# Performance work log

Measured on AMD Instinct MI355X. Metric: run time of the kernel, lower is better.

The kernel has to match this reference:

```python
import jax, jax.numpy as jnp
import numpy as np

K_TOP = 64  # top-k selection size (init kwarg k)


def setup_inputs() -> dict:
    key = jax.random.key(0)
    k1, k2, k3, k4 = jax.random.split(key, 4)
    N, M, D = 512, 100000, 1024
    queries = jax.random.normal(k1, (N, D), dtype=jnp.float32)
    keys = jax.random.normal(k2, (M, D), dtype=jnp.float32)
    values = jax.random.normal(k3, (M, D), dtype=jnp.float32)
    affine = jax.random.normal(k4, (D,), dtype=jnp.float32)  # diag affine param (low_parameter=True)
    return {"queries": queries, "keys": keys, "values": values, "affine": affine}


def reference(queries, keys, values, affine):
    # low_parameter=True -> weight matrix is diag(affine): (queries @ diag(a)) == queries * a
    # scores[n, m] = (queries * affine) @ keys.T ; reduce max over queries dim (dim=0)
    scores = jnp.max(jnp.einsum('nd,md->nm', queries * affine, keys), axis=0)  # [M]
    weights, indices = jax.lax.top_k(scores, K_TOP)            # [k], [k]
    w = jax.nn.softmax(weights)                                # softmax over the k selected scores
    encoding = jnp.sum(w[:, None] * values[indices], axis=0)   # [V]
    return encoding, indices
```

## Files before the change

kernel.cpp:

```cpp
#include <hip/hip_runtime.h>
#include <cstdint>
#include <cstddef>


typedef __attribute__((ext_vector_type(8))) short bf16x8;
typedef __attribute__((ext_vector_type(4))) float f32x4;

static constexpr int NQ = 512;
static constexpr int DD = 1024;
static constexpr int MK = 100000;
static constexpr int BM = 64;
static constexpr int BK = 64;
static constexpr int NKS = DD / BK;
static constexpr int MBLOCKS = (MK + BM - 1) / BM;
static constexpr int CAP = 1024;

static constexpr size_t QSTAGE_OFF   = 0;
static constexpr size_t QSTAGE_BYTES = (size_t)NKS * NQ * 128;
static constexpr size_t SCORES_OFF   = QSTAGE_OFF + QSTAGE_BYTES;
static constexpr size_t SCORES_BYTES = (size_t)MBLOCKS * BM * sizeof(float);
static constexpr size_t CIDX_OFF     = SCORES_OFF + SCORES_BYTES;
static constexpr size_t RESC_OFF     = CIDX_OFF + (size_t)CAP * 4;
static constexpr size_t CNT_OFF      = RESC_OFF + (size_t)CAP * 4;

static constexpr int A_HI = 0;
static constexpr int B_HI = 8192;
static constexpr int GEMM_LDS = 8192 + 65536;

static __device__ __forceinline__ unsigned short f32_to_bf16_rne(float f) {
    unsigned int u = __float_as_uint(f);
    unsigned int r = (u + 0x7FFFu + ((u >> 16) & 1u)) >> 16;
    return (unsigned short)r;
}

static __device__ __forceinline__ unsigned int xform(float f) {
    unsigned int u = __float_as_uint(f);
    return u ^ ((unsigned int)((int)u >> 31) | 0x80000000u);
}
static __device__ __forceinline__ float unxform(unsigned int u) {
    unsigned int b = (u & 0x80000000u) ? (u ^ 0x80000000u) : ~u;
    return __uint_as_float(b);
}

typedef __attribute__((address_space(1))) const unsigned int g1u32;
typedef __attribute__((address_space(3))) unsigned int l3u32;
static __device__ __forceinline__ void async16(const void* g, void* l) {
    __builtin_amdgcn_global_load_lds((g1u32*)g, (l3u32*)(uintptr_t)l, 16, 0, 0);
}

__global__ void prep_q(const float* __restrict__ q, const float* __restrict__ a,
                       unsigned short* __restrict__ qs) {
    int id  = blockIdx.x * 256 + threadIdx.x;
    int p   = id & 7;
    int row = (id >> 3) & (NQ - 1);
    int ks  = id >> 12;
    int c   = p ^ (row & 7);
    int kb  = ks * BK + c * 8;

    const float* qrow = q + (size_t)row * DD + kb;
    float4 v0 = *(const float4*)(qrow);
    float4 v1 = *(const float4*)(qrow + 4);
    float4 a0 = *(const float4*)(a + kb);
    float4 a1 = *(const float4*)(a + kb + 4);
    float f[8] = {v0.x * a0.x, v0.y * a0.y, v0.z * a0.z, v0.w * a0.w,
                  v1.x * a1.x, v1.y * a1.y, v1.z * a1.z, v1.w * a1.w};
    bf16x8 o;
#pragma unroll
    for (int j = 0; j < 8; ++j) o[j] = (short)f32_to_bf16_rne(f[j]);
    *(bf16x8*)(qs + (size_t)id * 8) = o;
}

__launch_bounds__(512, 4)
__global__ void scores_gemm(const float* __restrict__ keys,
                            const unsigned short* __restrict__ qs,
                            float* __restrict__ scores) {
    extern __shared__ char smem[];
    const int tid  = threadIdx.x;
    const int wid  = tid >> 6;
    const int lane = tid & 63;
    const int g    = lane >> 4;
    const int r16  = lane & 15;
    const int m0   = blockIdx.x * BM;

    f32x4 acc[4][4] = {};

    const int arow   = tid >> 3;
    const int acw    = tid & 7;
    const int abyte  = arow * 128 + ((acw ^ (arow & 7)) << 4);
    const bool avalid = (m0 + arow) < MK;
    const float* akey = keys + (size_t)(m0 + arow) * DD + acw * 8;

    char* bhi_dst = smem + B_HI + wid * 8192;
    const char* bsrc = (const char*)qs;

    for (int ks = 0; ks < NKS; ++ks) {
        const char* shi = bsrc + ((size_t)(ks * NQ + wid * 64)) * 128 + lane * 16;
#pragma unroll
        for (int i = 0; i < 8; ++i)
            async16(shi + i * 1024, bhi_dst + i * 1024);

        float f[8];
        if (avalid) {
            float4 v0 = *(const float4*)(akey + (size_t)ks * BK);
            float4 v1 = *(const float4*)(akey + (size_t)ks * BK + 4);
            f[0]=v0.x; f[1]=v0.y; f[2]=v0.z; f[3]=v0.w;
            f[4]=v1.x; f[5]=v1.y; f[6]=v1.z; f[7]=v1.w;
        } else {
#pragma unroll
            for (int j = 0; j < 8; ++j) f[j] = 0.f;
        }
        bf16x8 hi8;
#pragma unroll
        for (int j = 0; j < 8; ++j) hi8[j] = (short)f32_to_bf16_rne(f[j]);
        *(bf16x8*)(smem + A_HI + abyte) = hi8;

        __syncthreads();

#pragma unroll
        for (int s = 0; s < 2; ++s) {
            bf16x8 ah[4], bh[4];
#pragma unroll
            for (int rt = 0; rt < 4; ++rt) {
                int row  = rt * 16 + r16;
                int byte = row * 128 + (((s * 4 + g) ^ (row & 7)) << 4);
                ah[rt] = *(const bf16x8*)(smem + A_HI + byte);
            }
#pragma unroll
            for (int ct = 0; ct < 4; ++ct) {
                int row  = wid * 64 + ct * 16 + r16;
                int byte = row * 128 + (((s * 4 + g) ^ (row & 7)) << 4);
                bh[ct] = *(const bf16x8*)(smem + B_HI + byte);
            }
#pragma unroll
            for (int rt = 0; rt < 4; ++rt)
#pragma unroll
                for (int ct = 0; ct < 4; ++ct)
                    acc[rt][ct] = __builtin_amdgcn_mfma_f32_16x16x32_bf16(ah[rt], bh[ct], acc[rt][ct], 0, 0, 0);
        }
        __syncthreads();
    }

    float* wmax = (float*)smem;
#pragma unroll
    for (int rt = 0; rt < 4; ++rt) {
#pragma unroll
        for (int r = 0; r < 4; ++r) {
            float mx = acc[rt][0][r];
            mx = fmaxf(mx, acc[rt][1][r]);
            mx = fmaxf(mx, acc[rt][2][r]);
            mx = fmaxf(mx, acc[rt][3][r]);
#pragma unroll
            for (int off = 1; off < 16; off <<= 1)
                mx = fmaxf(mx, __shfl_xor(mx, off));
            if (r16 == 0) wmax[wid * 64 + rt * 16 + g * 4 + r] = mx;
        }
    }
    __syncthreads();
    if (tid < BM) {
        float mx = wmax[tid];
#pragma unroll
        for (int w = 1; w < 8; ++w) mx = fmaxf(mx, wmax[w * 64 + tid]);
        int gm = m0 + tid;
        if (gm < MK) scores[gm] = mx;
    }
}

__launch_bounds__(1024)
__global__ void finalize_select(const float* __restrict__ scores,
                                int* __restrict__ cidx, int* __restrict__ cnt) {
    __shared__ unsigned int hist[8192];
    __shared__ unsigned int csum[1024];
    __shared__ int sbT;
    __shared__ int scnt;
    const int tid = threadIdx.x;
    for (int i = tid; i < 8192; i += 1024) hist[i] = 0;
    if (tid == 0) scnt = 0;
    __syncthreads();

    for (int i = tid; i < MK; i += 1024)
        atomicAdd(&hist[xform(scores[i]) >> 19], 1u);
    __syncthreads();

    unsigned int s = 0;
#pragma unroll
    for (int j = 0; j < 8; ++j) s += hist[tid * 8 + j];
    csum[tid] = s;
    __syncthreads();

    if (tid == 0) {
        unsigned int acc = 0;
        int bT = 0;
        for (int cb = 1023; cb >= 0; --cb) {
            unsigned int c = csum[cb];
            if (acc + c >= 64u) {
                for (int b = cb * 8 + 7;; --b) {
                    acc += hist[b];
                    if (acc >= 64u) { bT = b; break; }
                }
                break;
            }
            acc += c;
        }
        sbT = bT;
    }
    __syncthreads();

    const float vlo = unxform((unsigned int)sbT << 19) - 1.0f;
    for (int i = tid; i < MK; i += 1024) {
        if (scores[i] >= vlo) {
            int p = atomicAdd(&scnt, 1);
            if (p < CAP) cidx[p] = i;
        }
    }
    __syncthreads();
    if (tid == 0) cnt[0] = scnt < CAP ? scnt : CAP;
}

__launch_bounds__(256)
__global__ void rescore(const float* __restrict__ q, const float* __restrict__ a,
                        const float* __restrict__ keys,
                        const int* __restrict__ cidx, const int* __restrict__ cnt,
                        float* __restrict__ resc) {
    __shared__ float w[1024];
    __shared__ float smax[4];
    const int b = blockIdx.x;
    if (b >= cnt[0]) return;
    const int m   = cidx[b];
    const int tid = threadIdx.x;

    for (int d = tid; d < 1024; d += 256) w[d] = a[d] * keys[(size_t)m * DD + d];
    __syncthreads();

    const int wid = tid >> 6, lane = tid & 63;
    float best = -__builtin_inff();
    for (int n = wid; n < NQ; n += 4) {
        const float* qr = q + (size_t)n * DD;
        float p = 0.f;
#pragma unroll
        for (int j = 0; j < 4; ++j) {
            float4 v  = *(const float4*)(qr + lane * 4 + 256 * j);
            float4 ww = *(const float4*)(&w[lane * 4 + 256 * j]);
            p += v.x * ww.x + v.y * ww.y + v.z * ww.z + v.w * ww.w;
        }
#pragma unroll
        for (int off = 1; off < 64; off <<= 1) p += __shfl_xor(p, off);
        best = fmaxf(best, p);
    }
    if (lane == 0) smax[wid] = best;
    __syncthreads();
    if (tid == 0)
        resc[b] = fmaxf(fmaxf(smax[0], smax[1]), fmaxf(smax[2], smax[3]));
}

__launch_bounds__(256)
__global__ void final_select(const int* __restrict__ cidx, const float* __restrict__ resc,
                             const int* __restrict__ cnt, const float* __restrict__ values,
                             float* __restrict__ out) {
    __shared__ float selw[64];
    __shared__ int   seli[64];
    const int tid = threadIdx.x;
    int nc = cnt[0];
    if (nc > CAP) nc = CAP;

    if (tid < 64) {
        const int lane = tid;
        float lv[16]; int li[16];
#pragma unroll
        for (int j = 0; j < 16; ++j) {
            int slot = lane + 64 * j;
            bool ok = slot < nc;
            lv[j] = ok ? resc[slot] : -__builtin_inff();
            li[j] = ok ? cidx[slot] : 0x7fffffff;
        }
        for (int it = 0; it < 64; ++it) {
            float bv = -__builtin_inff();
            int bg = 0x7fffffff, bj = 0;
#pragma unroll
            for (int j = 0; j < 16; ++j)
                if (lv[j] > bv || (lv[j] == bv && li[j] < bg)) { bv = lv[j]; bg = li[j]; bj = j; }
            int bcode = (lane << 4) | bj;
#pragma unroll
            for (int off = 1; off < 64; off <<= 1) {
                float ov = __shfl_xor(bv, off);
                int   og = __shfl_xor(bg, off);
                int   oc = __shfl_xor(bcode, off);
                if (ov > bv || (ov == bv && og < bg)) { bv = ov; bg = og; bcode = oc; }
            }
            if ((bcode >> 4) == lane) {
                int wj = bcode & 15;
#pragma unroll
                for (int j = 0; j < 16; ++j) if (j == wj) lv[j] = -__builtin_inff();
            }
            if (lane == 0) { selw[it] = bv; seli[it] = bg; }
        }
    }
    __syncthreads();

    if (tid < 64) {
        float x = selw[tid];
        float mx = x;
#pragma unroll
        for (int off = 1; off < 64; off <<= 1) mx = fmaxf(mx, __shfl_xor(mx, off));
        float e = expf(x - mx);
        float s = e;
#pragma unroll
        for (int off = 1; off < 64; off <<= 1) s += __shfl_xor(s, off);
        selw[tid] = e / s;
        out[DD + tid] = (float)seli[tid];
    }
    __syncthreads();

    for (int d = tid; d < DD; d += 256) {
        float accv = 0.f;
        for (int i = 0; i < 64; ++i)
            accv += selw[i] * values[(size_t)seli[i] * DD + d];
        out[d] = accv;
    }
}

extern "C" void kernel_launch(void* const* d_in, const int* in_sizes, int n_in,
                              void* d_out, int out_size, void* d_ws, size_t ws_size,
                              hipStream_t stream) {
    (void)in_sizes; (void)n_in; (void)out_size; (void)ws_size;
    const float* queries = (const float*)d_in[0];
    const float* keys    = (const float*)d_in[1];
    const float* values  = (const float*)d_in[2];
    const float* affine  = (const float*)d_in[3];
    float* out = (float*)d_out;
    char*  ws  = (char*)d_ws;

    unsigned short* qstage = (unsigned short*)(ws + QSTAGE_OFF);
    float* scores = (float*)(ws + SCORES_OFF);
    int*   cidx   = (int*)(ws + CIDX_OFF);
    float* resc   = (float*)(ws + RESC_OFF);
    int*   cnt    = (int*)(ws + CNT_OFF);

    hipFuncSetAttribute((const void*)scores_gemm,
                        hipFuncAttributeMaxDynamicSharedMemorySize, GEMM_LDS);

    prep_q<<<(NKS * NQ * 8) / 256, 256, 0, stream>>>(queries, affine, qstage);
    scores_gemm<<<MBLOCKS, 512, GEMM_LDS, stream>>>(keys, qstage, scores);
    finalize_select<<<1, 1024, 0, stream>>>(scores, cidx, cnt);
    rescore<<<CAP, 256, 0, stream>>>(queries, affine, keys, cidx, cnt, resc);
    final_select<<<1, 256, 0, stream>>>(cidx, resc, cnt, values, out);
}
```

Measured before the change: 498.0 us.

## Double-buffer score GEMM with prefetch and parallelize top-k threshold selection

The score GEMM halves its K-step to 32, double-buffers both the query tile and the bf16-converted key tile in LDS, and issues the next step's async and global loads before the current MFMAs. This leaves one barrier per step and raises wave priority around the MFMA block. The single-block select kernel is split into separate kernels: zeroing, a multi-block histogram build with global atomics, a parallel suffix-scan threshold search, and a multi-block candidate collect. The intent is to hide load latency in the GEMM and remove the serial one-block pass over 100k scores, at the cost of extra launches and global atomics. The candidate count is no longer clamped to CAP.

```diff
diff --git a/kernel.cpp b/kernel.cpp
--- a/kernel.cpp
+++ b/kernel.cpp
@@ -10,29 +10,30 @@
 static constexpr int DD = 1024;
 static constexpr int MK = 100000;
 static constexpr int BM = 64;
-static constexpr int BK = 64;
+static constexpr int BK = 32;
 static constexpr int NKS = DD / BK;
 static constexpr int MBLOCKS = (MK + BM - 1) / BM;
 static constexpr int CAP = 1024;
 
 static constexpr size_t QSTAGE_OFF   = 0;
-static constexpr size_t QSTAGE_BYTES = (size_t)NKS * NQ * 128;
+static constexpr size_t QSTAGE_BYTES = (size_t)NKS * NQ * 64;
 static constexpr size_t SCORES_OFF   = QSTAGE_OFF + QSTAGE_BYTES;
 static constexpr size_t SCORES_BYTES = (size_t)MBLOCKS * BM * sizeof(float);
 static constexpr size_t CIDX_OFF     = SCORES_OFF + SCORES_BYTES;
 static constexpr size_t RESC_OFF     = CIDX_OFF + (size_t)CAP * 4;
 static constexpr size_t CNT_OFF      = RESC_OFF + (size_t)CAP * 4;
-
-static constexpr int A_HI = 0;
-static constexpr int B_HI = 8192;
-static constexpr int GEMM_LDS = 8192 + 65536;
+static constexpr size_t HIST_OFF     = CNT_OFF + 64;
+static constexpr size_t VLO_OFF      = HIST_OFF + 8192 * 4;
+
+static constexpr int AOFF = 0;
+static constexpr int BOFF = 8192;
+static constexpr int GEMM_LDS = 8192 + 2 * 32768;
 
 static __device__ __forceinline__ unsigned short f32_to_bf16_rne(float f) {
     unsigned int u = __float_as_uint(f);
     unsigned int r = (u + 0x7FFFu + ((u >> 16) & 1u)) >> 16;
     return (unsigned short)r;
 }
-
 static __device__ __forceinline__ unsigned int xform(float f) {
     unsigned int u = __float_as_uint(f);
     return u ^ ((unsigned int)((int)u >> 31) | 0x80000000u);
@@ -40,6 +41,9 @@
 static __device__ __forceinline__ float unxform(unsigned int u) {
     unsigned int b = (u & 0x80000000u) ? (u ^ 0x80000000u) : ~u;
     return __uint_as_float(b);
+}
+static __device__ __forceinline__ int swz4(int row) {
+    return ((row >> 2) ^ row) & 3;
 }
 
 typedef __attribute__((address_space(1))) const unsigned int g1u32;
@@ -51,11 +55,10 @@
 __global__ void prep_q(const float* __restrict__ q, const float* __restrict__ a,
                        unsigned short* __restrict__ qs) {
     int id  = blockIdx.x * 256 + threadIdx.x;
-    int p   = id & 7;
-    int row = (id >> 3) & (NQ - 1);
-    int ks  = id >> 12;
-    int c   = p ^ (row & 7);
-    int kb  = ks * BK + c * 8;
+    int c   = id & 3;
+    int row = (id >> 2) & (NQ - 1);
+    int ks  = id >> 11;
+    int kb  = ks * BK + (c ^ swz4(row)) * 8;
 
     const float* qrow = q + (size_t)row * DD + kb;
     float4 v0 = *(const float4*)(qrow);
@@ -82,63 +85,91 @@
     const int r16  = lane & 15;
     const int m0   = blockIdx.x * BM;
 
+    const int arow = tid >> 3;
+    const int ah   = tid & 7;
+    int srowA = (m0 + arow < MK) ? (m0 + arow) : (MK - 1);
+    const float* aptr = keys + (size_t)srowA * DD + ah * 4;
+    const int awbyte = arow * 64 + ((((ah >> 1) ^ swz4(arow)) & 3) << 4) + (ah & 1) * 8;
+
+    const char* bsrc = (const char*)qs + (size_t)(wid * 64) * 64 + (size_t)lane * 16;
+    const int bdst0 = BOFF + wid * 4096;
+
+    int aoff[4], boff[4];
+#pragma unroll
+    for (int rt = 0; rt < 4; ++rt) {
+        int row = rt * 16 + r16;
+        aoff[rt] = row * 64 + (((g ^ swz4(row)) & 3) << 4);
+    }
+#pragma unroll
+    for (int ct = 0; ct < 4; ++ct) {
+        int row = wid * 64 + ct * 16 + r16;
+        boff[ct] = row * 64 + (((g ^ swz4(row)) & 3) << 4);
+    }
+
     f32x4 acc[4][4] = {};
 
-    const int arow   = tid >> 3;
-    const int acw    = tid & 7;
-    const int abyte  = arow * 128 + ((acw ^ (arow & 7)) << 4);
-    const bool avalid = (m0 + arow) < MK;
-    const float* akey = keys + (size_t)(m0 + arow) * DD + acw * 8;
-
-    char* bhi_dst = smem + B_HI + wid * 8192;
-    const char* bsrc = (const char*)qs;
-
-    for (int ks = 0; ks < NKS; ++ks) {
-        const char* shi = bsrc + ((size_t)(ks * NQ + wid * 64)) * 128 + lane * 16;
-#pragma unroll
-        for (int i = 0; i < 8; ++i)
-            async16(shi + i * 1024, bhi_dst + i * 1024);
-
-        float f[8];
-        if (avalid) {
-            float4 v0 = *(const float4*)(akey + (size_t)ks * BK);
-            float4 v1 = *(const float4*)(akey + (size_t)ks * BK + 4);
-            f[0]=v0.x; f[1]=v0.y; f[2]=v0.z; f[3]=v0.w;
-            f[4]=v1.x; f[5]=v1.y; f[6]=v1.z; f[7]=v1.w;
-        } else {
-#pragma unroll
-            for (int j = 0; j < 8; ++j) f[j] = 0.f;
-        }
-        bf16x8 hi8;
-#pragma unroll
-        for (int j = 0; j < 8; ++j) hi8[j] = (short)f32_to_bf16_rne(f[j]);
-        *(bf16x8*)(smem + A_HI + abyte) = hi8;
-
+#pragma unroll
+    for (int j = 0; j < 4; ++j)
+        async16(bsrc + j * 1024, smem + bdst0 + j * 1024);
+    {
+        float4 a0 = *(const float4*)(aptr);
+        unsigned long long pk =
+            (unsigned long long)f32_to_bf16_rne(a0.x)
+          | ((unsigned long long)f32_to_bf16_rne(a0.y) << 16)
+          | ((unsigned long long)f32_to_bf16_rne(a0.z) << 32)
+          | ((unsigned long long)f32_to_bf16_rne(a0.w) << 48);
+        *(unsigned long long*)(smem + AOFF + awbyte) = pk;
+    }
+    __syncthreads();
+
+    for (int ks = 0; ks < NKS - 1; ++ks) {
+        const int cur = ks & 1, nxt = cur ^ 1;
+#pragma unroll
+        for (int j = 0; j < 4; ++j)
+            async16(bsrc + (size_t)(ks + 1) * 32768 + j * 1024,
+                    smem + bdst0 + nxt * 32768 + j * 1024);
+        float4 an = *(const float4*)(aptr + (ks + 1) * BK);
+
+        bf16x8 ah4[4], bh4[4];
+#pragma unroll
+        for (int rt = 0; rt < 4; ++rt)
+            ah4[rt] = *(const bf16x8*)(smem + AOFF + cur * 4096 + aoff[rt]);
+#pragma unroll
+        for (int ct = 0; ct < 4; ++ct)
+            bh4[ct] = *(const bf16x8*)(smem + BOFF + cur * 32768 + boff[ct]);
+        __builtin_amdgcn_s_setprio(1);
+#pragma unroll
+        for (int rt = 0; rt < 4; ++rt)
+#pragma unroll
+            for (int ct = 0; ct < 4; ++ct)
+                acc[rt][ct] = __builtin_amdgcn_mfma_f32_16x16x32_bf16(ah4[rt], bh4[ct], acc[rt][ct], 0, 0, 0);
+        __builtin_amdgcn_s_setprio(0);
+
+        unsigned long long pk =
+            (unsigned long long)f32_to_bf16_rne(an.x)
+          | ((unsigned long long)f32_to_bf16_rne(an.y) << 16)
+          | ((unsigned long long)f32_to_bf16_rne(an.z) << 32)
+          | ((unsigned long long)f32_to_bf16_rne(an.w) << 48);
+        *(unsigned long long*)(smem + AOFF + nxt * 4096 + awbyte) = pk;
         __syncthreads();
-
-#pragma unroll
-        for (int s = 0; s < 2; ++s) {
-            bf16x8 ah[4], bh[4];
-#pragma unroll
-            for (int rt = 0; rt < 4; ++rt) {
-                int row  = rt * 16 + r16;
-                int byte = row * 128 + (((s * 4 + g) ^ (row & 7)) << 4);
-                ah[rt] = *(const bf16x8*)(smem + A_HI + byte);
-            }
-#pragma unroll
-            for (int ct = 0; ct < 4; ++ct) {
-                int row  = wid * 64 + ct * 16 + r16;
-                int byte = row * 128 + (((s * 4 + g) ^ (row & 7)) << 4);
-                bh[ct] = *(const bf16x8*)(smem + B_HI + byte);
-            }
-#pragma unroll
-            for (int rt = 0; rt < 4; ++rt)
-#pragma unroll
-                for (int ct = 0; ct < 4; ++ct)
-                    acc[rt][ct] = __builtin_amdgcn_mfma_f32_16x16x32_bf16(ah[rt], bh[ct], acc[rt][ct], 0, 0, 0);
-        }
-        __syncthreads();
-    }
+    }
+
+    {
+        const int cur = (NKS - 1) & 1;
+        bf16x8 ah4[4], bh4[4];
+#pragma unroll
+        for (int rt = 0; rt < 4; ++rt)
+            ah4[rt] = *(const bf16x8*)(smem + AOFF + cur * 4096 + aoff[rt]);
+#pragma unroll
+        for (int ct = 0; ct < 4; ++ct)
+            bh4[ct] = *(const bf16x8*)(smem + BOFF + cur * 32768 + boff[ct]);
+#pragma unroll
+        for (int rt = 0; rt < 4; ++rt)
+#pragma unroll
+            for (int ct = 0; ct < 4; ++ct)
+                acc[rt][ct] = __builtin_amdgcn_mfma_f32_16x16x32_bf16(ah4[rt], bh4[ct], acc[rt][ct], 0, 0, 0);
+    }
+    __syncthreads();
 
     float* wmax = (float*)smem;
 #pragma unroll
@@ -165,55 +196,54 @@
     }
 }
 
+__global__ void zero_hist(unsigned int* __restrict__ hist, int* __restrict__ cnt) {
+    int i = blockIdx.x * 1024 + threadIdx.x;
+    if (i < 8192) hist[i] = 0;
+    if (i == 0) cnt[0] = 0;
+}
+
+__global__ void hist_build(const float* __restrict__ scores, unsigned int* __restrict__ hist) {
+    for (int i = blockIdx.x * 256 + threadIdx.x; i < MK; i += gridDim.x * 256)
+        atomicAdd(&hist[xform(scores[i]) >> 19], 1u);
+}
+
 __launch_bounds__(1024)
-__global__ void finalize_select(const float* __restrict__ scores,
-                                int* __restrict__ cidx, int* __restrict__ cnt) {
-    __shared__ unsigned int hist[8192];
-    __shared__ unsigned int csum[1024];
-    __shared__ int sbT;
-    __shared__ int scnt;
+__global__ void find_thresh(const unsigned int* __restrict__ hist, float* __restrict__ vlo) {
+    __shared__ unsigned int s0[1024], s1[1024];
     const int tid = threadIdx.x;
-    for (int i = tid; i < 8192; i += 1024) hist[i] = 0;
-    if (tid == 0) scnt = 0;
-    __syncthreads();
-
-    for (int i = tid; i < MK; i += 1024)
-        atomicAdd(&hist[xform(scores[i]) >> 19], 1u);
-    __syncthreads();
-
     unsigned int s = 0;
 #pragma unroll
     for (int j = 0; j < 8; ++j) s += hist[tid * 8 + j];
-    csum[tid] = s;
-    __syncthreads();
-
-    if (tid == 0) {
-        unsigned int acc = 0;
-        int bT = 0;
-        for (int cb = 1023; cb >= 0; --cb) {
-            unsigned int c = csum[cb];
-            if (acc + c >= 64u) {
-                for (int b = cb * 8 + 7;; --b) {
-                    acc += hist[b];
-                    if (acc >= 64u) { bT = b; break; }
-                }
-                break;
-            }
-            acc += c;
-        }
-        sbT = bT;
-    }
-    __syncthreads();
-
-    const float vlo = unxform((unsigned int)sbT << 19) - 1.0f;
-    for (int i = tid; i < MK; i += 1024) {
-        if (scores[i] >= vlo) {
-            int p = atomicAdd(&scnt, 1);
+    s0[tid] = s;
+    __syncthreads();
+    unsigned int* src = s0;
+    unsigned int* dst = s1;
+    for (int off = 1; off < 1024; off <<= 1) {
+        unsigned int v = src[tid] + ((tid + off < 1024) ? src[tid + off] : 0u);
+        __syncthreads();
+        dst[tid] = v;
+        __syncthreads();
+        unsigned int* t = src; src = dst; dst = t;
+    }
+    unsigned int suf  = src[tid];
+    unsigned int sufn = (tid < 1023) ? src[tid + 1] : 0u;
+    if (suf >= 64u && sufn < 64u) {
+        unsigned int acc = sufn;
+        int b = tid * 8 + 7;
+        for (;; --b) { acc += hist[b]; if (acc >= 64u) break; }
+        vlo[0] = unxform(((unsigned int)b) << 19) - 1.0f;
+    }
+}
+
+__global__ void collect(const float* __restrict__ scores, const float* __restrict__ vlo,
+                        int* __restrict__ cidx, int* __restrict__ cnt) {
+    const float t = vlo[0];
+    for (int i = blockIdx.x * 256 + threadIdx.x; i < MK; i += gridDim.x * 256) {
+        if (scores[i] >= t) {
+            int p = atomicAdd(cnt, 1);
             if (p < CAP) cidx[p] = i;
         }
     }
-    __syncthreads();
-    if (tid == 0) cnt[0] = scnt < CAP ? scnt : CAP;
 }
 
 __launch_bounds__(256)
@@ -334,13 +364,18 @@
     int*   cidx   = (int*)(ws + CIDX_OFF);
     float* resc   = (float*)(ws + RESC_OFF);
     int*   cnt    = (int*)(ws + CNT_OFF);
+    unsigned int* hist = (unsigned int*)(ws + HIST_OFF);
+    float* vlo    = (float*)(ws + VLO_OFF);
 
     hipFuncSetAttribute((const void*)scores_gemm,
                         hipFuncAttributeMaxDynamicSharedMemorySize, GEMM_LDS);
 
-    prep_q<<<(NKS * NQ * 8) / 256, 256, 0, stream>>>(queries, affine, qstage);
+    prep_q<<<(NKS * NQ * 4) / 256, 256, 0, stream>>>(queries, affine, qstage);
     scores_gemm<<<MBLOCKS, 512, GEMM_LDS, stream>>>(keys, qstage, scores);
-    finalize_select<<<1, 1024, 0, stream>>>(scores, cidx, cnt);
+    zero_hist<<<8, 1024, 0, stream>>>(hist, cnt);
+    hist_build<<<200, 256, 0, stream>>>(scores, hist);
+    find_thresh<<<1, 1024, 0, stream>>>(hist, vlo);
+    collect<<<200, 256, 0, stream>>>(scores, vlo, cidx, cnt);
     rescore<<<CAP, 256, 0, stream>>>(queries, affine, keys, cidx, cnt, resc);
     final_select<<<1, 256, 0, stream>>>(cidx, resc, cnt, values, out);
 }
```

New measurement: 793.4 us. 1.59x slower.
